# Kernel tuning notes

Measured on AMD Instinct MI355X. Metric: run time of the kernel, lower is better.

The kernel has to match this reference:

```python
import jax, jax.numpy as jnp
import numpy as np

N, E, F0, HEADS, B, OUT = 100000, 1600000, 128, 4, 64, 32
CHANNELS = [16, 8, 4, 2]
NEG_SLOPE = 0.2


def setup_inputs() -> dict:
    key = jax.random.key(0)
    ks = jax.random.split(key, 40)
    inp = {}
    inp['x'] = jax.random.normal(ks[0], (N, F0), dtype=jnp.float32)
    inp['edge_index'] = jax.random.randint(ks[1], (2, E), 0, N, dtype=jnp.int64)
    inp['batch'] = jnp.sort(jax.random.randint(ks[2], (N,), 0, B, dtype=jnp.int64))
    # GATConv params per layer: W [in, heads*out], att_src/att_dst [heads, out], bias [heads*out]
    in_dim = F0
    ki = 3
    for li, oc in enumerate(CHANNELS, start=1):
        scale = 1.0 / np.sqrt(in_dim)
        inp[f'W{li}'] = jax.random.normal(ks[ki], (in_dim, HEADS * oc), dtype=jnp.float32) * scale
        inp[f'a_src{li}'] = jax.random.normal(ks[ki + 1], (HEADS, oc), dtype=jnp.float32) * 0.1
        inp[f'a_dst{li}'] = jax.random.normal(ks[ki + 2], (HEADS, oc), dtype=jnp.float32) * 0.1
        inp[f'b{li}'] = jnp.zeros((HEADS * oc,), dtype=jnp.float32)
        ki += 3
        in_dim = HEADS * oc
    inp['W_fc'] = jax.random.normal(ks[ki], (2 * HEADS, OUT), dtype=jnp.float32) * (1.0 / np.sqrt(2 * HEADS))
    inp['b_fc'] = jnp.zeros((OUT,), dtype=jnp.float32)
    return inp


def gat_layer(x, src, dst, W, a_src, a_dst, b, oc):
    n = x.shape[0]
    h = (x @ W).reshape(n, HEADS, oc)                    # [N, H, C]
    al_s = jnp.einsum('nhc,hc->nh', h, a_src)            # [N, H]
    al_d = jnp.einsum('nhc,hc->nh', h, a_dst)
    e = jax.nn.leaky_relu(al_s[src] + al_d[dst], NEG_SLOPE)  # [E, H]
    # segment softmax over incoming edges per destination node
    m = jax.ops.segment_max(e, dst, num_segments=n)
    m = jnp.where(jnp.isfinite(m), m, 0.0)
    ex = jnp.exp(e - m[dst])
    s = jax.ops.segment_sum(ex, dst, num_segments=n)
    alpha = ex / (s[dst] + 1e-16)                        # [E, H]
    out = jax.ops.segment_sum(h[src] * alpha[:, :, None], dst, num_segments=n)
    return out.reshape(n, HEADS * oc) + b


def reference(x, edge_index, batch, W1, a_src1, a_dst1, b1, W2, a_src2, a_dst2, b2,
              W3, a_src3, a_dst3, b3, W4, a_src4, a_dst4, b4, W_fc, b_fc):
    n = x.shape[0]
    loops = jnp.arange(n, dtype=edge_index.dtype)
    src = jnp.concatenate([edge_index[0], loops])   # PyG GATConv adds self-loops
    dst = jnp.concatenate([edge_index[1], loops])
    params = [(W1, a_src1, a_dst1, b1), (W2, a_src2, a_dst2, b2),
              (W3, a_src3, a_dst3, b3), (W4, a_src4, a_dst4, b4)]
    h = x
    for (W, a_s, a_d, b), oc in zip(params, CHANNELS):
        h = jax.nn.relu(gat_layer(h, src, dst, W, a_s, a_d, b, oc))
        # dropout(0.3) is identity at inference
    # global mean pool over graphs in the batch
    sums = jax.ops.segment_sum(h, batch, num_segments=B)
    cnt = jax.ops.segment_sum(jnp.ones((n,), h.dtype), batch, num_segments=B)
    pooled = sums / jnp.maximum(cnt, 1.0)[:, None]
    return pooled @ W_fc + b_fc
```

## Files before the change

### kernel.cpp

```cpp
#include <hip/hip_runtime.h>
#include <hip/hip_bf16.h>

#define NNODES 100000
#define NEDGES 1600000
#define NHEADS 4
#define NGRAPH 64
#define NOUTF  32
#define BSH    9
#define NBUK   ((NNODES + 511) >> 9)
#define BPAD   16
#define BCAP   9216
#define CGRID  512
#define G1GRID ((NNODES + 63) / 64)

__device__ __forceinline__ unsigned short f2bf(float f) {
    union { float f; unsigned u; } v;
    v.f = f;
    unsigned r = v.u + 0x7FFF + ((v.u >> 16) & 1);
    return (unsigned short)(r >> 16);
}
__device__ __forceinline__ float bflo(unsigned u) {
    union { unsigned u; float f; } v;
    v.u = u << 16;
    return v.f;
}
__device__ __forceinline__ float bfhi(unsigned u) {
    union { unsigned u; float f; } v;
    v.u = u & 0xFFFF0000u;
    return v.f;
}

__device__ __forceinline__ bool ei_is_int64(const int* __restrict__ ei) {
    int acc = 0;
    #pragma unroll
    for (int i = 0; i < 32; i++) acc |= ei[2 * i + 1];
    return acc == 0;
}

__device__ __forceinline__ void fma4(float4& a, float s, const float4& b) {
    a.x += s * b.x;
    a.y += s * b.y;
    a.z += s * b.z;
    a.w += s * b.w;
}

__global__ __launch_bounds__(256) void gat_coarse_gemm1_kernel(
        const int* __restrict__ ei, const int* __restrict__ bt,
        int* __restrict__ bkcur, int* __restrict__ packed, int* __restrict__ bat,
        const float* __restrict__ x, const float* __restrict__ W1,
        const float* __restrict__ as1, const float* __restrict__ ad1,
        unsigned short* __restrict__ h1, float* __restrict__ al_s,
        float* __restrict__ al_d, int ne, int n) {
    __shared__ float smem[64 * 64 + 64 * 132];
    const int tid = threadIdx.x;
    if (blockIdx.x < CGRID) {
        int* hist = (int*)smem;
        int* base = hist + NBUK;
        for (int i = tid; i < NBUK; i += 256) hist[i] = 0;
        __syncthreads();
        bool wide = ei_is_int64(ei);
        int chunk = (ne + CGRID - 1) / CGRID;
        int e0 = blockIdx.x * chunk;
        int e1 = min(e0 + chunk, ne);
        for (int i = e0 + tid; i < e1; i += 256) {
            int d = wide ? ei[2 * (ne + i)] : ei[ne + i];
            atomicAdd(&hist[d >> BSH], 1);
        }
        __syncthreads();
        for (int i = tid; i < NBUK; i += 256)
            base[i] = hist[i] ? atomicAdd(&bkcur[i * BPAD], hist[i]) : 0;
        __syncthreads();
        for (int i = tid; i < NBUK; i += 256) hist[i] = 0;
        __syncthreads();
        for (int i = e0 + tid; i < e1; i += 256) {
            int s = wide ? ei[2 * i] : ei[i];
            int d = wide ? ei[2 * (ne + i)] : ei[ne + i];
            int bk = d >> BSH;
            int pos = base[bk] + atomicAdd(&hist[bk], 1);
            if (pos < BCAP) packed[bk * BCAP + pos] = s | ((d & 511) << 17);
        }
        int gid = blockIdx.x * 256 + tid;
        for (int i = gid; i < n; i += CGRID * 256) bat[i] = wide ? bt[2 * i] : bt[i];
    } else {
        constexpr int DIN = 128, DOUT = 64, KTILE = 64;
        constexpr int OG = DOUT / 4;
        constexpr int NPB = 64;
        constexpr int S = DIN + 4;
        constexpr int C = DOUT / NHEADS;
        float* Wl = smem;
        float* xs = smem + KTILE * DOUT;
        const int base = (blockIdx.x - CGRID) * NPB;
        constexpr int KC = DIN / 4;
        for (int i = tid; i < NPB * KC; i += 256) {
            int nn = i / KC, kc = i - nn * KC;
            int nd = base + nn;
            float4 v = (nd < n) ? ((const float4*)x)[(size_t)nd * KC + kc]
                                : make_float4(0.f, 0.f, 0.f, 0.f);
            *(float4*)&xs[nn * S + kc * 4] = v;
        }
        const int og = tid % OG;
        const int ng = tid / OG;
        const int n0 = ng * 4;
        float4 acc[4] = {};
        for (int kt = 0; kt < DIN; kt += KTILE) {
            __syncthreads();
            for (int i = tid; i < KTILE * OG; i += 256)
                ((float4*)Wl)[i] = ((const float4*)W1)[kt * OG + i];
            __syncthreads();
            #pragma unroll 2
            for (int k = 0; k < KTILE; k += 4) {
                float4 wv[4], xv[4];
                #pragma unroll
                for (int j = 0; j < 4; j++)
                    wv[j] = *(const float4*)&Wl[(k + j) * DOUT + og * 4];
                #pragma unroll
                for (int r = 0; r < 4; r++)
                    xv[r] = *(const float4*)&xs[(n0 + r) * S + kt + k];
                #pragma unroll
                for (int r = 0; r < 4; r++) {
                    fma4(acc[r], xv[r].x, wv[0]);
                    fma4(acc[r], xv[r].y, wv[1]);
                    fma4(acc[r], xv[r].z, wv[2]);
                    fma4(acc[r], xv[r].w, wv[3]);
                }
            }
        }
        float4 asv = ((const float4*)as1)[og];
        float4 adv = ((const float4*)ad1)[og];
        #pragma unroll
        for (int r = 0; r < 4; r++) {
            int node = base + n0 + r;
            bool ok = node < n;
            if (ok) {
                ushort4 o;
                o.x = f2bf(acc[r].x);
                o.y = f2bf(acc[r].y);
                o.z = f2bf(acc[r].z);
                o.w = f2bf(acc[r].w);
                ((ushort4*)h1)[(size_t)node * OG + og] = o;
            }
            float ps = acc[r].x * asv.x + acc[r].y * asv.y + acc[r].z * asv.z + acc[r].w * asv.w;
            float pd = acc[r].x * adv.x + acc[r].y * adv.y + acc[r].z * adv.z + acc[r].w * adv.w;
            #pragma unroll
            for (int off = 1; off < C / 4; off <<= 1) {
                ps += __shfl_xor(ps, off);
                pd += __shfl_xor(pd, off);
            }
            if (ok && (og % (C / 4)) == 0) {
                int hh = og / (C / 4);
                al_s[node * NHEADS + hh] = ps;
                al_d[node * NHEADS + hh] = pd;
            }
        }
    }
}

__global__ __launch_bounds__(256) void gat_fine_kernel(
        const int* __restrict__ packed, const int* __restrict__ bkcur,
        int* __restrict__ row_ptr, int* __restrict__ col, int n) {
    __shared__ int bscan[256];
    __shared__ int dg[512];
    __shared__ int excl[512];
    __shared__ int partial[256];
    __shared__ int cur[512];
    int b = blockIdx.x;
    int tid = threadIdx.x;
    int c = (tid < NBUK) ? bkcur[tid * BPAD] : 0;
    bscan[tid] = c;
    __syncthreads();
    for (int off = 1; off < 256; off <<= 1) {
        int u = (tid >= off) ? bscan[tid - off] : 0;
        __syncthreads();
        bscan[tid] += u;
        __syncthreads();
    }
    int cntb = bkcur[b * BPAD];
    int csr0 = bscan[b] - cntb;
    for (int i = tid; i < 512; i += 256) dg[i] = 0;
    __syncthreads();
    int pbeg = b * BCAP;
    int pend = pbeg + cntb;
    for (int t = pbeg + tid; t < pend; t += 256)
        atomicAdd(&dg[packed[t] >> 17], 1);
    __syncthreads();
    int a0 = dg[2 * tid], a1 = dg[2 * tid + 1];
    int s = a0 + a1;
    partial[tid] = s;
    __syncthreads();
    for (int off = 1; off < 256; off <<= 1) {
        int u = (tid >= off) ? partial[tid - off] : 0;
        __syncthreads();
        partial[tid] += u;
        __syncthreads();
    }
    int ebase = partial[tid] - s;
    excl[2 * tid] = ebase;
    excl[2 * tid + 1] = ebase + a0;
    cur[2 * tid] = ebase;
    cur[2 * tid + 1] = ebase + a0;
    __syncthreads();
    int node0 = b << BSH;
    for (int i = tid; i < 512; i += 256) {
        int nd = node0 + i;
        if (nd < n) row_ptr[nd] = csr0 + excl[i];
    }
    if (b == NBUK - 1 && tid == 0) row_ptr[n] = bscan[NBUK - 1];
    for (int t = pbeg + tid; t < pend; t += 256) {
        int v = packed[t];
        int pos = atomicAdd(&cur[v >> 17], 1);
        col[csr0 + pos] = v & 0x1FFFF;
    }
}

template<int DIN, int DOUT, int KTILE, bool BF16OUT>
__global__ __launch_bounds__(256) void gat_gemm_attn_kernel(
        const float* __restrict__ in, const float* __restrict__ W,
        const float* __restrict__ a_src, const float* __restrict__ a_dst,
        void* __restrict__ hout, float* __restrict__ al_s, float* __restrict__ al_d, int n) {
    constexpr int OG = DOUT / 4;
    constexpr int NPB = 1024 / OG;
    constexpr int S = DIN + 4;
    constexpr int C = DOUT / NHEADS;
    __shared__ float Wl[KTILE * DOUT];
    __shared__ float xs[NPB * S];
    const int tid = threadIdx.x;
    const int base = blockIdx.x * NPB;
    constexpr int KC = DIN / 4;
    for (int i = tid; i < NPB * KC; i += 256) {
        int nn = i / KC, kc = i - nn * KC;
        int nd = base + nn;
        float4 v = (nd < n) ? ((const float4*)in)[(size_t)nd * KC + kc]
                            : make_float4(0.f, 0.f, 0.f, 0.f);
        *(float4*)&xs[nn * S + kc * 4] = v;
    }
    const int og = tid % OG;
    const int ng = tid / OG;
    const int n0 = ng * 4;
    float4 acc[4] = {};
    for (int kt = 0; kt < DIN; kt += KTILE) {
        __syncthreads();
        for (int i = tid; i < KTILE * OG; i += 256)
            ((float4*)Wl)[i] = ((const float4*)W)[kt * OG + i];
        __syncthreads();
        #pragma unroll 2
        for (int k = 0; k < KTILE; k += 4) {
            float4 wv[4], xv[4];
            #pragma unroll
            for (int j = 0; j < 4; j++)
                wv[j] = *(const float4*)&Wl[(k + j) * DOUT + og * 4];
            #pragma unroll
            for (int r = 0; r < 4; r++)
                xv[r] = *(const float4*)&xs[(n0 + r) * S + kt + k];
            #pragma unroll
            for (int r = 0; r < 4; r++) {
                fma4(acc[r], xv[r].x, wv[0]);
                fma4(acc[r], xv[r].y, wv[1]);
                fma4(acc[r], xv[r].z, wv[2]);
                fma4(acc[r], xv[r].w, wv[3]);
            }
        }
    }
    float4 asv = ((const float4*)a_src)[og];
    float4 adv = ((const float4*)a_dst)[og];
    #pragma unroll
    for (int r = 0; r < 4; r++) {
        int node = base + n0 + r;
        bool ok = node < n;
        if (ok) {
            if constexpr (BF16OUT) {
                ushort4 o;
                o.x = f2bf(acc[r].x);
                o.y = f2bf(acc[r].y);
                o.z = f2bf(acc[r].z);
                o.w = f2bf(acc[r].w);
                ((ushort4*)hout)[(size_t)node * OG + og] = o;
            } else {
                ((float4*)hout)[(size_t)node * OG + og] = acc[r];
            }
        }
        if constexpr (C >= 4) {
            float ps = acc[r].x * asv.x + acc[r].y * asv.y + acc[r].z * asv.z + acc[r].w * asv.w;
            float pd = acc[r].x * adv.x + acc[r].y * adv.y + acc[r].z * adv.z + acc[r].w * adv.w;
            #pragma unroll
            for (int off = 1; off < C / 4; off <<= 1) {
                ps += __shfl_xor(ps, off);
                pd += __shfl_xor(pd, off);
            }
            if (ok && (og % (C / 4)) == 0) {
                int hh = og / (C / 4);
                al_s[node * NHEADS + hh] = ps;
                al_d[node * NHEADS + hh] = pd;
            }
        } else {
            if (ok) {
                al_s[node * NHEADS + 2 * og]     = acc[r].x * asv.x + acc[r].y * asv.y;
                al_s[node * NHEADS + 2 * og + 1] = acc[r].z * asv.z + acc[r].w * asv.w;
                al_d[node * NHEADS + 2 * og]     = acc[r].x * adv.x + acc[r].y * adv.y;
                al_d[node * NHEADS + 2 * og + 1] = acc[r].z * adv.z + acc[r].w * adv.w;
            }
        }
    }
}

template<int C>
__global__ __launch_bounds__(256) void gat_agg_bf16_kernel(
        const unsigned short* __restrict__ h, const float* __restrict__ al_s,
        const float* __restrict__ al_d, const int* __restrict__ row_ptr,
        const int* __restrict__ col, const float* __restrict__ bias,
        float* __restrict__ out, int n) {
    constexpr int G = NHEADS * C;
    constexpr int L = G / 8;
    constexpr int NG = 64 / L;
    int lane = threadIdx.x & 63;
    int node = blockIdx.x * 4 + (threadIdx.x >> 6);
    if (node >= n) return;
    int sub = lane & (L - 1);
    int g = lane / L;
    int hh = (sub * 8) / C;
    int beg = row_ptr[node];
    int cnt = row_ptr[node + 1] - beg;
    float ald = al_d[node * NHEADS + hh];
    const uint4* h4 = (const uint4*)h;
    float a[8] = {};
    float ws = 0.f;
    for (int t = g; t < cnt + 1; t += NG) {
        int src = (t < cnt) ? col[beg + t] : node;
        float e = al_s[src * NHEADS + hh] + ald;
        e = (e > 0.f) ? e : 0.2f * e;
        float w = __expf(e);
        uint4 hv = h4[(size_t)src * L + sub];
        ws += w;
        a[0] += w * bflo(hv.x);
        a[1] += w * bfhi(hv.x);
        a[2] += w * bflo(hv.y);
        a[3] += w * bfhi(hv.y);
        a[4] += w * bflo(hv.z);
        a[5] += w * bfhi(hv.z);
        a[6] += w * bflo(hv.w);
        a[7] += w * bfhi(hv.w);
    }
    #pragma unroll
    for (int off = L; off < 64; off <<= 1) {
        #pragma unroll
        for (int k = 0; k < 8; k++) a[k] += __shfl_xor(a[k], off);
        ws += __shfl_xor(ws, off);
    }
    if (g == 0) {
        float inv = 1.f / (ws + 1e-16f);
        int j0 = sub * 8;
        float4 o0, o1;
        float4 bv0 = *(const float4*)&bias[j0];
        float4 bv1 = *(const float4*)&bias[j0 + 4];
        o0.x = a[0] * inv + bv0.x;
        o0.y = a[1] * inv + bv0.y;
        o0.z = a[2] * inv + bv0.z;
        o0.w = a[3] * inv + bv0.w;
        o1.x = a[4] * inv + bv1.x;
        o1.y = a[5] * inv + bv1.y;
        o1.z = a[6] * inv + bv1.z;
        o1.w = a[7] * inv + bv1.w;
        o0.x = (o0.x > 0.f) ? o0.x : 0.f;
        o0.y = (o0.y > 0.f) ? o0.y : 0.f;
        o0.z = (o0.z > 0.f) ? o0.z : 0.f;
        o0.w = (o0.w > 0.f) ? o0.w : 0.f;
        o1.x = (o1.x > 0.f) ? o1.x : 0.f;
        o1.y = (o1.y > 0.f) ? o1.y : 0.f;
        o1.z = (o1.z > 0.f) ? o1.z : 0.f;
        o1.w = (o1.w > 0.f) ? o1.w : 0.f;
        *(float4*)&out[(size_t)node * G + j0] = o0;
        *(float4*)&out[(size_t)node * G + j0 + 4] = o1;
    }
}

__global__ __launch_bounds__(256) void gat_agg_bf16_c4_kernel(
        const unsigned short* __restrict__ h, const float* __restrict__ al_s,
        const float* __restrict__ al_d, const int* __restrict__ row_ptr,
        const int* __restrict__ col, const float* __restrict__ bias,
        float* __restrict__ out, int n) {
    constexpr int G = 16;
    constexpr int L = 4;
    constexpr int NG = 16;
    int lane = threadIdx.x & 63;
    int node = blockIdx.x * 4 + (threadIdx.x >> 6);
    if (node >= n) return;
    int sub = lane & (L - 1);
    int g = lane / L;
    int beg = row_ptr[node];
    int cnt = row_ptr[node + 1] - beg;
    float ald = al_d[node * NHEADS + sub];
    const uint2* h2 = (const uint2*)h;
    float a[4] = {};
    float ws = 0.f;
    for (int t = g; t < cnt + 1; t += NG) {
        int src = (t < cnt) ? col[beg + t] : node;
        float e = al_s[src * NHEADS + sub] + ald;
        e = (e > 0.f) ? e : 0.2f * e;
        float w = __expf(e);
        uint2 hv = h2[(size_t)src * L + sub];
        ws += w;
        a[0] += w * bflo(hv.x);
        a[1] += w * bfhi(hv.x);
        a[2] += w * bflo(hv.y);
        a[3] += w * bfhi(hv.y);
    }
    #pragma unroll
    for (int off = L; off < 64; off <<= 1) {
        #pragma unroll
        for (int k = 0; k < 4; k++) a[k] += __shfl_xor(a[k], off);
        ws += __shfl_xor(ws, off);
    }
    if (g == 0) {
        float inv = 1.f / (ws + 1e-16f);
        int j0 = sub * 4;
        float4 bv = *(const float4*)&bias[j0];
        float4 o;
        o.x = a[0] * inv + bv.x;
        o.y = a[1] * inv + bv.y;
        o.z = a[2] * inv + bv.z;
        o.w = a[3] * inv + bv.w;
        o.x = (o.x > 0.f) ? o.x : 0.f;
        o.y = (o.y > 0.f) ? o.y : 0.f;
        o.z = (o.z > 0.f) ? o.z : 0.f;
        o.w = (o.w > 0.f) ? o.w : 0.f;
        *(float4*)&out[(size_t)node * G + j0] = o;
    }
}

template<int C>
__global__ __launch_bounds__(256) void gat_agg_kernel(
        const float* __restrict__ h, const float* __restrict__ al_s, const float* __restrict__ al_d,
        const int* __restrict__ row_ptr, const int* __restrict__ col,
        const float* __restrict__ bias, float* __restrict__ out, int n) {
    constexpr int G = NHEADS * C;
    constexpr int L = G / 4;
    constexpr int NG = 64 / L;
    int lane = threadIdx.x & 63;
    int node = blockIdx.x * 4 + (threadIdx.x >> 6);
    if (node >= n) return;
    int sub = lane & (L - 1);
    int g = lane / L;
    int c0 = sub * 4;
    int beg = row_ptr[node];
    int cnt = row_ptr[node + 1] - beg;
    float ald0 = al_d[node * NHEADS + c0 / C];
    float ald1 = al_d[node * NHEADS + (c0 + 2) / C];
    const float4* h4 = (const float4*)h;
    float4 acc = make_float4(0.f, 0.f, 0.f, 0.f);
    float ws0 = 0.f, ws1 = 0.f;
    for (int t = g; t < cnt + 1; t += NG) {
        int src = (t < cnt) ? col[beg + t] : node;
        float4 hv = h4[src * L + sub];
        float e0 = al_s[src * NHEADS + c0 / C] + ald0;
        float e1 = al_s[src * NHEADS + (c0 + 2) / C] + ald1;
        e0 = (e0 > 0.f) ? e0 : 0.2f * e0;
        e1 = (e1 > 0.f) ? e1 : 0.2f * e1;
        float w0 = __expf(e0);
        float w1 = __expf(e1);
        ws0 += w0;
        ws1 += w1;
        acc.x += w0 * hv.x;
        acc.y += w0 * hv.y;
        acc.z += w1 * hv.z;
        acc.w += w1 * hv.w;
    }
    #pragma unroll
    for (int off = L; off < 64; off <<= 1) {
        acc.x += __shfl_xor(acc.x, off);
        acc.y += __shfl_xor(acc.y, off);
        acc.z += __shfl_xor(acc.z, off);
        acc.w += __shfl_xor(acc.w, off);
        ws0 += __shfl_xor(ws0, off);
        ws1 += __shfl_xor(ws1, off);
    }
    if (g == 0) {
        float4 bv = ((const float4*)bias)[sub];
        float4 v;
        v.x = acc.x / (ws0 + 1e-16f) + bv.x;
        v.y = acc.y / (ws0 + 1e-16f) + bv.y;
        v.z = acc.z / (ws1 + 1e-16f) + bv.z;
        v.w = acc.w / (ws1 + 1e-16f) + bv.w;
        v.x = (v.x > 0.f) ? v.x : 0.f;
        v.y = (v.y > 0.f) ? v.y : 0.f;
        v.z = (v.z > 0.f) ? v.z : 0.f;
        v.w = (v.w > 0.f) ? v.w : 0.f;
        ((float4*)out)[node * L + sub] = v;
    }
}

__global__ __launch_bounds__(256) void gat_poolfc_kernel(
        const float* __restrict__ x, const int* __restrict__ bat,
        const float* __restrict__ Wfc, const float* __restrict__ bfc,
        float* __restrict__ out, int n) {
    __shared__ float sh[256][9];
    int b = blockIdx.x;
    int tid = threadIdx.x;
    int lo = 0, hi = n;
    while (lo < hi) { int mid = (lo + hi) >> 1; if (bat[mid] < b) lo = mid + 1; else hi = mid; }
    int i0 = lo;
    hi = n;
    while (lo < hi) { int mid = (lo + hi) >> 1; if (bat[mid] < b + 1) lo = mid + 1; else hi = mid; }
    int i1 = lo;
    float a[8] = {};
    for (int i = i0 + tid; i < i1; i += 256) {
        float4 v0 = ((const float4*)x)[(size_t)i * 2];
        float4 v1 = ((const float4*)x)[(size_t)i * 2 + 1];
        a[0] += v0.x; a[1] += v0.y; a[2] += v0.z; a[3] += v0.w;
        a[4] += v1.x; a[5] += v1.y; a[6] += v1.z; a[7] += v1.w;
    }
    #pragma unroll
    for (int k = 0; k < 8; k++) sh[tid][k] = a[k];
    __syncthreads();
    for (int off = 128; off >= 1; off >>= 1) {
        if (tid < off)
            #pragma unroll
            for (int k = 0; k < 8; k++) sh[tid][k] += sh[tid + off][k];
        __syncthreads();
    }
    if (tid < NOUTF) {
        float c = (float)(i1 - i0);
        if (c < 1.f) c = 1.f;
        float acc = bfc[tid];
        #pragma unroll
        for (int d = 0; d < 8; d++) acc += (sh[0][d] / c) * Wfc[d * NOUTF + tid];
        out[b * NOUTF + tid] = acc;
    }
}

extern "C" void kernel_launch(void* const* d_in, const int* in_sizes, int n_in,
                              void* d_out, int out_size, void* d_ws, size_t ws_size,
                              hipStream_t stream) {
    const float* x = (const float*)d_in[0];
    const int* ei = (const int*)d_in[1];
    const int* batch = (const int*)d_in[2];
    const float* W1 = (const float*)d_in[3];
    const float* as1 = (const float*)d_in[4];
    const float* ad1 = (const float*)d_in[5];
    const float* b1 = (const float*)d_in[6];
    const float* W2 = (const float*)d_in[7];
    const float* as2 = (const float*)d_in[8];
    const float* ad2 = (const float*)d_in[9];
    const float* b2 = (const float*)d_in[10];
    const float* W3 = (const float*)d_in[11];
    const float* as3 = (const float*)d_in[12];
    const float* ad3 = (const float*)d_in[13];
    const float* b3 = (const float*)d_in[14];
    const float* W4 = (const float*)d_in[15];
    const float* as4 = (const float*)d_in[16];
    const float* ad4 = (const float*)d_in[17];
    const float* b4 = (const float*)d_in[18];
    const float* Wfc = (const float*)d_in[19];
    const float* bfc = (const float*)d_in[20];

    const int n = NNODES, ne = NEDGES;

    char* p = (char*)d_ws;
    auto carve = [&](size_t bytes) {
        char* r = p;
        p += (bytes + 255) & ~(size_t)255;
        return r;
    };
    int* row_ptr = (int*)carve((size_t)(n + 1) * 4);
    int* col = (int*)carve((size_t)ne * 4);
    int* bkcur = (int*)carve(256 * BPAD * 4);
    int* packed = (int*)carve((size_t)NBUK * BCAP * 4);
    float* buf_h = (float*)carve((size_t)n * 64 * 4);
    float* buf_x = (float*)carve((size_t)n * 64 * 4);
    float* al_s = (float*)carve((size_t)n * NHEADS * 4);
    float* al_d = (float*)carve((size_t)n * NHEADS * 4);
    int* bat = (int*)carve((size_t)n * 4);
    unsigned short* h_bf16 = (unsigned short*)buf_h;

    hipMemsetAsync(bkcur, 0, 256 * BPAD * 4, stream);

    gat_coarse_gemm1_kernel<<<CGRID + G1GRID, 256, 0, stream>>>(
        ei, batch, bkcur, packed, bat, x, W1, as1, ad1, h_bf16, al_s, al_d, ne, n);

    gat_fine_kernel<<<NBUK, 256, 0, stream>>>(packed, bkcur, row_ptr, col, n);

    gat_agg_bf16_kernel<16><<<(n + 3) / 4, 256, 0, stream>>>(
        h_bf16, al_s, al_d, row_ptr, col, b1, buf_x, n);

    gat_gemm_attn_kernel<64, 32, 64, true><<<(n + 127) / 128, 256, 0, stream>>>(
        buf_x, W2, as2, ad2, h_bf16, al_s, al_d, n);
    gat_agg_bf16_kernel<8><<<(n + 3) / 4, 256, 0, stream>>>(
        h_bf16, al_s, al_d, row_ptr, col, b2, buf_x, n);

    gat_gemm_attn_kernel<32, 16, 32, true><<<(n + 255) / 256, 256, 0, stream>>>(
        buf_x, W3, as3, ad3, h_bf16, al_s, al_d, n);
    gat_agg_bf16_c4_kernel<<<(n + 3) / 4, 256, 0, stream>>>(
        h_bf16, al_s, al_d, row_ptr, col, b3, buf_x, n);

    gat_gemm_attn_kernel<16, 8, 16, false><<<(n + 511) / 512, 256, 0, stream>>>(
        buf_x, W4, as4, ad4, buf_h, al_s, al_d, n);
    gat_agg_kernel<2><<<(n + 3) / 4, 256, 0, stream>>>(buf_h, al_s, al_d, row_ptr, col, b4, buf_x, n);

    gat_poolfc_kernel<<<NGRAPH, 256, 0, stream>>>(buf_x, bat, Wfc, bfc, (float*)d_out, n);
}
```

Baseline: 409.1 us.

## Map aggregation to thread groups per node and widen CSR fine kernel

The aggregation kernels now give each destination node a small group of lanes (L lanes covering the feature row), so a wave handles many nodes, instead of one wave per node with an edge-parallel shuffle reduction. Each lane walks all incoming edges itself, two per iteration, which removes the cross-lane shuffle reductions and the idle lanes on low-degree nodes. The cost is serial per-lane loops, so high-degree nodes cause imbalance and divergence within a wave. The fine CSR build kernel also goes to 1024 threads to speed up its histogram and scatter loops.

```diff
diff --git a/kernel.cpp b/kernel.cpp
--- a/kernel.cpp
+++ b/kernel.cpp
@@ -155,7 +155,7 @@
     }
 }
 
-__global__ __launch_bounds__(256) void gat_fine_kernel(
+__global__ __launch_bounds__(1024) void gat_fine_kernel(
         const int* __restrict__ packed, const int* __restrict__ bkcur,
         int* __restrict__ row_ptr, int* __restrict__ col, int n) {
     __shared__ int bscan[256];
@@ -165,47 +165,51 @@
     __shared__ int cur[512];
     int b = blockIdx.x;
     int tid = threadIdx.x;
-    int c = (tid < NBUK) ? bkcur[tid * BPAD] : 0;
-    bscan[tid] = c;
+    if (tid < 256) bscan[tid] = (tid < NBUK) ? bkcur[tid * BPAD] : 0;
+    if (tid < 512) dg[tid] = 0;
     __syncthreads();
     for (int off = 1; off < 256; off <<= 1) {
-        int u = (tid >= off) ? bscan[tid - off] : 0;
-        __syncthreads();
-        bscan[tid] += u;
+        int u = (tid < 256 && tid >= off) ? bscan[tid - off] : 0;
+        __syncthreads();
+        if (tid < 256) bscan[tid] += u;
         __syncthreads();
     }
     int cntb = bkcur[b * BPAD];
     int csr0 = bscan[b] - cntb;
-    for (int i = tid; i < 512; i += 256) dg[i] = 0;
-    __syncthreads();
     int pbeg = b * BCAP;
     int pend = pbeg + cntb;
-    for (int t = pbeg + tid; t < pend; t += 256)
+    for (int t = pbeg + tid; t < pend; t += 1024)
         atomicAdd(&dg[packed[t] >> 17], 1);
     __syncthreads();
-    int a0 = dg[2 * tid], a1 = dg[2 * tid + 1];
-    int s = a0 + a1;
-    partial[tid] = s;
+    int a0 = 0, a1 = 0, s = 0;
+    if (tid < 256) {
+        a0 = dg[2 * tid];
+        a1 = dg[2 * tid + 1];
+        s = a0 + a1;
+        partial[tid] = s;
+    }
     __syncthreads();
     for (int off = 1; off < 256; off <<= 1) {
-        int u = (tid >= off) ? partial[tid - off] : 0;
-        __syncthreads();
-        partial[tid] += u;
-        __syncthreads();
-    }
-    int ebase = partial[tid] - s;
-    excl[2 * tid] = ebase;
-    excl[2 * tid + 1] = ebase + a0;
-    cur[2 * tid] = ebase;
-    cur[2 * tid + 1] = ebase + a0;
+        int u = (tid < 256 && tid >= off) ? partial[tid - off] : 0;
+        __syncthreads();
+        if (tid < 256) partial[tid] += u;
+        __syncthreads();
+    }
+    if (tid < 256) {
+        int ebase = partial[tid] - s;
+        excl[2 * tid] = ebase;
+        excl[2 * tid + 1] = ebase + a0;
+        cur[2 * tid] = ebase;
+        cur[2 * tid + 1] = ebase + a0;
+    }
     __syncthreads();
     int node0 = b << BSH;
-    for (int i = tid; i < 512; i += 256) {
-        int nd = node0 + i;
-        if (nd < n) row_ptr[nd] = csr0 + excl[i];
+    if (tid < 512) {
+        int nd = node0 + tid;
+        if (nd < n) row_ptr[nd] = csr0 + excl[tid];
     }
     if (b == NBUK - 1 && tid == 0) row_ptr[n] = bscan[NBUK - 1];
-    for (int t = pbeg + tid; t < pend; t += 256) {
+    for (int t = pbeg + tid; t < pend; t += 1024) {
         int v = packed[t];
         int pos = atomicAdd(&cur[v >> 17], 1);
         col[csr0 + pos] = v & 0x1FFFF;
@@ -302,189 +306,243 @@
     }
 }
 
-template<int C>
-__global__ __launch_bounds__(256) void gat_agg_bf16_kernel(
+template<int G>
+__global__ __launch_bounds__(256) void gat_agg_group_kernel(
         const unsigned short* __restrict__ h, const float* __restrict__ al_s,
         const float* __restrict__ al_d, const int* __restrict__ row_ptr,
         const int* __restrict__ col, const float* __restrict__ bias,
         float* __restrict__ out, int n) {
-    constexpr int G = NHEADS * C;
     constexpr int L = G / 8;
-    constexpr int NG = 64 / L;
+    constexpr int PW = 64 / L;
+    constexpr int C = G / NHEADS;
     int lane = threadIdx.x & 63;
-    int node = blockIdx.x * 4 + (threadIdx.x >> 6);
+    int sub = lane & (L - 1);
+    int gidx = lane / L;
+    int node = blockIdx.x * (4 * PW) + (threadIdx.x >> 6) * PW + gidx;
     if (node >= n) return;
-    int sub = lane & (L - 1);
-    int g = lane / L;
-    int hh = (sub * 8) / C;
     int beg = row_ptr[node];
     int cnt = row_ptr[node + 1] - beg;
-    float ald = al_d[node * NHEADS + hh];
     const uint4* h4 = (const uint4*)h;
-    float a[8] = {};
-    float ws = 0.f;
-    for (int t = g; t < cnt + 1; t += NG) {
-        int src = (t < cnt) ? col[beg + t] : node;
-        float e = al_s[src * NHEADS + hh] + ald;
-        e = (e > 0.f) ? e : 0.2f * e;
-        float w = __expf(e);
-        uint4 hv = h4[(size_t)src * L + sub];
-        ws += w;
-        a[0] += w * bflo(hv.x);
-        a[1] += w * bfhi(hv.x);
-        a[2] += w * bflo(hv.y);
-        a[3] += w * bfhi(hv.y);
-        a[4] += w * bflo(hv.z);
-        a[5] += w * bfhi(hv.z);
-        a[6] += w * bflo(hv.w);
-        a[7] += w * bfhi(hv.w);
-    }
-    #pragma unroll
-    for (int off = L; off < 64; off <<= 1) {
+    float acc[8] = {};
+    int j0 = sub * 8;
+    if constexpr (C >= 8) {
+        const int hh = (sub * 8) / C;
+        float ald = al_d[node * NHEADS + hh];
+        float ws = 0.f;
+        int total = cnt + 1;
+        int t = 0;
+        for (; t + 2 <= total; t += 2) {
+            int s0 = col[beg + t];
+            int s1 = (t + 1 < cnt) ? col[beg + t + 1] : node;
+            float e0 = al_s[s0 * NHEADS + hh] + ald;
+            float e1 = al_s[s1 * NHEADS + hh] + ald;
+            uint4 hv0 = h4[(size_t)s0 * L + sub];
+            uint4 hv1 = h4[(size_t)s1 * L + sub];
+            e0 = (e0 > 0.f) ? e0 : 0.2f * e0;
+            e1 = (e1 > 0.f) ? e1 : 0.2f * e1;
+            float w0 = __expf(e0);
+            float w1 = __expf(e1);
+            ws += w0;
+            acc[0] += w0 * bflo(hv0.x);
+            acc[1] += w0 * bfhi(hv0.x);
+            acc[2] += w0 * bflo(hv0.y);
+            acc[3] += w0 * bfhi(hv0.y);
+            acc[4] += w0 * bflo(hv0.z);
+            acc[5] += w0 * bfhi(hv0.z);
+            acc[6] += w0 * bflo(hv0.w);
+            acc[7] += w0 * bfhi(hv0.w);
+            ws += w1;
+            acc[0] += w1 * bflo(hv1.x);
+            acc[1] += w1 * bfhi(hv1.x);
+            acc[2] += w1 * bflo(hv1.y);
+            acc[3] += w1 * bfhi(hv1.y);
+            acc[4] += w1 * bflo(hv1.z);
+            acc[5] += w1 * bfhi(hv1.z);
+            acc[6] += w1 * bflo(hv1.w);
+            acc[7] += w1 * bfhi(hv1.w);
+        }
+        if (t < total) {
+            int s0 = (t < cnt) ? col[beg + t] : node;
+            float e0 = al_s[s0 * NHEADS + hh] + ald;
+            uint4 hv0 = h4[(size_t)s0 * L + sub];
+            e0 = (e0 > 0.f) ? e0 : 0.2f * e0;
+            float w0 = __expf(e0);
+            ws += w0;
+            acc[0] += w0 * bflo(hv0.x);
+            acc[1] += w0 * bfhi(hv0.x);
+            acc[2] += w0 * bflo(hv0.y);
+            acc[3] += w0 * bfhi(hv0.y);
+            acc[4] += w0 * bflo(hv0.z);
+            acc[5] += w0 * bfhi(hv0.z);
+            acc[6] += w0 * bflo(hv0.w);
+            acc[7] += w0 * bfhi(hv0.w);
+        }
+        float inv = 1.f / (ws + 1e-16f);
         #pragma unroll
-        for (int k = 0; k < 8; k++) a[k] += __shfl_xor(a[k], off);
-        ws += __shfl_xor(ws, off);
-    }
-    if (g == 0) {
-        float inv = 1.f / (ws + 1e-16f);
-        int j0 = sub * 8;
-        float4 o0, o1;
-        float4 bv0 = *(const float4*)&bias[j0];
-        float4 bv1 = *(const float4*)&bias[j0 + 4];
-        o0.x = a[0] * inv + bv0.x;
-        o0.y = a[1] * inv + bv0.y;
-        o0.z = a[2] * inv + bv0.z;
-        o0.w = a[3] * inv + bv0.w;
-        o1.x = a[4] * inv + bv1.x;
-        o1.y = a[5] * inv + bv1.y;
-        o1.z = a[6] * inv + bv1.z;
-        o1.w = a[7] * inv + bv1.w;
-        o0.x = (o0.x > 0.f) ? o0.x : 0.f;
-        o0.y = (o0.y > 0.f) ? o0.y : 0.f;
-        o0.z = (o0.z > 0.f) ? o0.z : 0.f;
-        o0.w = (o0.w > 0.f) ? o0.w : 0.f;
-        o1.x = (o1.x > 0.f) ? o1.x : 0.f;
-        o1.y = (o1.y > 0.f) ? o1.y : 0.f;
-        o1.z = (o1.z > 0.f) ? o1.z : 0.f;
-        o1.w = (o1.w > 0.f) ? o1.w : 0.f;
-        *(float4*)&out[(size_t)node * G + j0] = o0;
-        *(float4*)&out[(size_t)node * G + j0 + 4] = o1;
-    }
-}
-
-__global__ __launch_bounds__(256) void gat_agg_bf16_c4_kernel(
-        const unsigned short* __restrict__ h, const float* __restrict__ al_s,
-        const float* __restrict__ al_d, const int* __restrict__ row_ptr,
-        const int* __restrict__ col, const float* __restrict__ bias,
-        float* __restrict__ out, int n) {
-    constexpr int G = 16;
-    constexpr int L = 4;
-    constexpr int NG = 16;
-    int lane = threadIdx.x & 63;
-    int node = blockIdx.x * 4 + (threadIdx.x >> 6);
-    if (node >= n) return;
-    int sub = lane & (L - 1);
-    int g = lane / L;
-    int beg = row_ptr[node];
-    int cnt = row_ptr[node + 1] - beg;
-    float ald = al_d[node * NHEADS + sub];
-    const uint2* h2 = (const uint2*)h;
-    float a[4] = {};
-    float ws = 0.f;
-    for (int t = g; t < cnt + 1; t += NG) {
-        int src = (t < cnt) ? col[beg + t] : node;
-        float e = al_s[src * NHEADS + sub] + ald;
-        e = (e > 0.f) ? e : 0.2f * e;
-        float w = __expf(e);
-        uint2 hv = h2[(size_t)src * L + sub];
-        ws += w;
-        a[0] += w * bflo(hv.x);
-        a[1] += w * bfhi(hv.x);
-        a[2] += w * bflo(hv.y);
-        a[3] += w * bfhi(hv.y);
-    }
-    #pragma unroll
-    for (int off = L; off < 64; off <<= 1) {
+        for (int k = 0; k < 8; k++) acc[k] = acc[k] * inv + bias[j0 + k];
+    } else {
+        const int hh0 = 2 * sub, hh1 = 2 * sub + 1;
+        float ald0 = al_d[node * NHEADS + hh0];
+        float ald1 = al_d[node * NHEADS + hh1];
+        float ws0 = 0.f, ws1 = 0.f;
+        int total = cnt + 1;
+        int t = 0;
+        for (; t + 2 <= total; t += 2) {
+            int s0 = col[beg + t];
+            int s1 = (t + 1 < cnt) ? col[beg + t + 1] : node;
+            float e00 = al_s[s0 * NHEADS + hh0] + ald0;
+            float e01 = al_s[s0 * NHEADS + hh1] + ald1;
+            float e10 = al_s[s1 * NHEADS + hh0] + ald0;
+            float e11 = al_s[s1 * NHEADS + hh1] + ald1;
+            uint4 hv0 = h4[(size_t)s0 * L + sub];
+            uint4 hv1 = h4[(size_t)s1 * L + sub];
+            e00 = (e00 > 0.f) ? e00 : 0.2f * e00;
+            e01 = (e01 > 0.f) ? e01 : 0.2f * e01;
+            e10 = (e10 > 0.f) ? e10 : 0.2f * e10;
+            e11 = (e11 > 0.f) ? e11 : 0.2f * e11;
+            float w00 = __expf(e00);
+            float w01 = __expf(e01);
+            float w10 = __expf(e10);
+            float w11 = __expf(e11);
+            ws0 += w00;
+            ws1 += w01;
+            acc[0] += w00 * bflo(hv0.x);
+            acc[1] += w00 * bfhi(hv0.x);
+            acc[2] += w00 * bflo(hv0.y);
+            acc[3] += w00 * bfhi(hv0.y);
+            acc[4] += w01 * bflo(hv0.z);
+            acc[5] += w01 * bfhi(hv0.z);
+            acc[6] += w01 * bflo(hv0.w);
+            acc[7] += w01 * bfhi(hv0.w);
+            ws0 += w10;
+            ws1 += w11;
+            acc[0] += w10 * bflo(hv1.x);
+            acc[1] += w10 * bfhi(hv1.x);
+            acc[2] += w10 * bflo(hv1.y);
+            acc[3] += w10 * bfhi(hv1.y);
+            acc[4] += w11 * bflo(hv1.z);
+            acc[5] += w11 * bfhi(hv1.z);
+            acc[6] += w11 * bflo(hv1.w);
+            acc[7] += w11 * bfhi(hv1.w);
+        }
+        if (t < total) {
+            int s0 = (t < cnt) ? col[beg + t] : node;
+            float e00 = al_s[s0 * NHEADS + hh0] + ald0;
+            float e01 = al_s[s0 * NHEADS + hh1] + ald1;
+            uint4 hv0 = h4[(size_t)s0 * L + sub];
+            e00 = (e00 > 0.f) ? e00 : 0.2f * e00;
+            e01 = (e01 > 0.f) ? e01 : 0.2f * e01;
+            float w00 = __expf(e00);
+            float w01 = __expf(e01);
+            ws0 += w00;
+            ws1 += w01;
+            acc[0] += w00 * bflo(hv0.x);
+            acc[1] += w00 * bfhi(hv0.x);
+            acc[2] += w00 * bflo(hv0.y);
+            acc[3] += w00 * bfhi(hv0.y);
+            acc[4] += w01 * bflo(hv0.z);
+            acc[5] += w01 * bfhi(hv0.z);
+            acc[6] += w01 * bflo(hv0.w);
+            acc[7] += w01 * bfhi(hv0.w);
+        }
+        float inv0 = 1.f / (ws0 + 1e-16f);
+        float inv1 = 1.f / (ws1 + 1e-16f);
         #pragma unroll
-        for (int k = 0; k < 4; k++) a[k] += __shfl_xor(a[k], off);
-        ws += __shfl_xor(ws, off);
-    }
-    if (g == 0) {
-        float inv = 1.f / (ws + 1e-16f);
-        int j0 = sub * 4;
-        float4 bv = *(const float4*)&bias[j0];
-        float4 o;
-        o.x = a[0] * inv + bv.x;
-        o.y = a[1] * inv + bv.y;
-        o.z = a[2] * inv + bv.z;
-        o.w = a[3] * inv + bv.w;
-        o.x = (o.x > 0.f) ? o.x : 0.f;
-        o.y = (o.y > 0.f) ? o.y : 0.f;
-        o.z = (o.z > 0.f) ? o.z : 0.f;
-        o.w = (o.w > 0.f) ? o.w : 0.f;
-        *(float4*)&out[(size_t)node * G + j0] = o;
-    }
-}
-
-template<int C>
-__global__ __launch_bounds__(256) void gat_agg_kernel(
+        for (int k = 0; k < 4; k++) acc[k] = acc[k] * inv0 + bias[j0 + k];
+        #pragma unroll
+        for (int k = 4; k < 8; k++) acc[k] = acc[k] * inv1 + bias[j0 + k];
+    }
+    float4 o0, o1;
+    o0.x = (acc[0] > 0.f) ? acc[0] : 0.f;
+    o0.y = (acc[1] > 0.f) ? acc[1] : 0.f;
+    o0.z = (acc[2] > 0.f) ? acc[2] : 0.f;
+    o0.w = (acc[3] > 0.f) ? acc[3] : 0.f;
+    o1.x = (acc[4] > 0.f) ? acc[4] : 0.f;
+    o1.y = (acc[5] > 0.f) ? acc[5] : 0.f;
+    o1.z = (acc[6] > 0.f) ? acc[6] : 0.f;
+    o1.w = (acc[7] > 0.f) ? acc[7] : 0.f;
+    *(float4*)&out[(size_t)node * G + j0] = o0;
+    *(float4*)&out[(size_t)node * G + j0 + 4] = o1;
+}
+
+__global__ __launch_bounds__(256) void gat_agg_f32_group_kernel(
         const float* __restrict__ h, const float* __restrict__ al_s, const float* __restrict__ al_d,
         const int* __restrict__ row_ptr, const int* __restrict__ col,
         const float* __restrict__ bias, float* __restrict__ out, int n) {
-    constexpr int G = NHEADS * C;
-    constexpr int L = G / 4;
-    constexpr int NG = 64 / L;
+    constexpr int L = 2;
+    constexpr int PW = 32;
     int lane = threadIdx.x & 63;
-    int node = blockIdx.x * 4 + (threadIdx.x >> 6);
+    int sub = lane & 1;
+    int gidx = lane >> 1;
+    int node = blockIdx.x * (4 * PW) + (threadIdx.x >> 6) * PW + gidx;
     if (node >= n) return;
-    int sub = lane & (L - 1);
-    int g = lane / L;
-    int c0 = sub * 4;
     int beg = row_ptr[node];
     int cnt = row_ptr[node + 1] - beg;
-    float ald0 = al_d[node * NHEADS + c0 / C];
-    float ald1 = al_d[node * NHEADS + (c0 + 2) / C];
+    const int hh0 = 2 * sub, hh1 = 2 * sub + 1;
+    float ald0 = al_d[node * NHEADS + hh0];
+    float ald1 = al_d[node * NHEADS + hh1];
     const float4* h4 = (const float4*)h;
     float4 acc = make_float4(0.f, 0.f, 0.f, 0.f);
     float ws0 = 0.f, ws1 = 0.f;
-    for (int t = g; t < cnt + 1; t += NG) {
-        int src = (t < cnt) ? col[beg + t] : node;
-        float4 hv = h4[src * L + sub];
-        float e0 = al_s[src * NHEADS + c0 / C] + ald0;
-        float e1 = al_s[src * NHEADS + (c0 + 2) / C] + ald1;
-        e0 = (e0 > 0.f) ? e0 : 0.2f * e0;
-        e1 = (e1 > 0.f) ? e1 : 0.2f * e1;
-        float w0 = __expf(e0);
-        float w1 = __expf(e1);
-        ws0 += w0;
-        ws1 += w1;
-        acc.x += w0 * hv.x;
-        acc.y += w0 * hv.y;
-        acc.z += w1 * hv.z;
-        acc.w += w1 * hv.w;
-    }
-    #pragma unroll
-    for (int off = L; off < 64; off <<= 1) {
-        acc.x += __shfl_xor(acc.x, off);
-        acc.y += __shfl_xor(acc.y, off);
-        acc.z += __shfl_xor(acc.z, off);
-        acc.w += __shfl_xor(acc.w, off);
-        ws0 += __shfl_xor(ws0, off);
-        ws1 += __shfl_xor(ws1, off);
-    }
-    if (g == 0) {
-        float4 bv = ((const float4*)bias)[sub];
-        float4 v;
-        v.x = acc.x / (ws0 + 1e-16f) + bv.x;
-        v.y = acc.y / (ws0 + 1e-16f) + bv.y;
-        v.z = acc.z / (ws1 + 1e-16f) + bv.z;
-        v.w = acc.w / (ws1 + 1e-16f) + bv.w;
-        v.x = (v.x > 0.f) ? v.x : 0.f;
-        v.y = (v.y > 0.f) ? v.y : 0.f;
-        v.z = (v.z > 0.f) ? v.z : 0.f;
-        v.w = (v.w > 0.f) ? v.w : 0.f;
-        ((float4*)out)[node * L + sub] = v;
-    }
+    int total = cnt + 1;
+    int t = 0;
+    for (; t + 2 <= total; t += 2) {
+        int s0 = col[beg + t];
+        int s1 = (t + 1 < cnt) ? col[beg + t + 1] : node;
+        float e00 = al_s[s0 * NHEADS + hh0] + ald0;
+        float e01 = al_s[s0 * NHEADS + hh1] + ald1;
+        float e10 = al_s[s1 * NHEADS + hh0] + ald0;
+        float e11 = al_s[s1 * NHEADS + hh1] + ald1;
+        float4 hv0 = h4[(size_t)s0 * L + sub];
+        float4 hv1 = h4[(size_t)s1 * L + sub];
+        e00 = (e00 > 0.f) ? e00 : 0.2f * e00;
+        e01 = (e01 > 0.f) ? e01 : 0.2f * e01;
+        e10 = (e10 > 0.f) ? e10 : 0.2f * e10;
+        e11 = (e11 > 0.f) ? e11 : 0.2f * e11;
+        float w00 = __expf(e00);
+        float w01 = __expf(e01);
+        float w10 = __expf(e10);
+        float w11 = __expf(e11);
+        ws0 += w00;
+        ws1 += w01;
+        acc.x += w00 * hv0.x;
+        acc.y += w00 * hv0.y;
+        acc.z += w01 * hv0.z;
+        acc.w += w01 * hv0.w;
+        ws0 += w10;
+        ws1 += w11;
+        acc.x += w10 * hv1.x;
+        acc.y += w10 * hv1.y;
+        acc.z += w11 * hv1.z;
+        acc.w += w11 * hv1.w;
+    }
+    if (t < total) {
+        int s0 = (t < cnt) ? col[beg + t] : node;
+        float e00 = al_s[s0 * NHEADS + hh0] + ald0;
+        float e01 = al_s[s0 * NHEADS + hh1] + ald1;
+        float4 hv0 = h4[(size_t)s0 * L + sub];
+        e00 = (e00 > 0.f) ? e00 : 0.2f * e00;
+        e01 = (e01 > 0.f) ? e01 : 0.2f * e01;
+        float w00 = __expf(e00);
+        float w01 = __expf(e01);
+        ws0 += w00;
+        ws1 += w01;
+        acc.x += w00 * hv0.x;
+        acc.y += w00 * hv0.y;
+        acc.z += w01 * hv0.z;
+        acc.w += w01 * hv0.w;
+    }
+    float4 bv = ((const float4*)bias)[sub];
+    float4 v;
+    v.x = acc.x / (ws0 + 1e-16f) + bv.x;
+    v.y = acc.y / (ws0 + 1e-16f) + bv.y;
+    v.z = acc.z / (ws1 + 1e-16f) + bv.z;
+    v.w = acc.w / (ws1 + 1e-16f) + bv.w;
+    v.x = (v.x > 0.f) ? v.x : 0.f;
+    v.y = (v.y > 0.f) ? v.y : 0.f;
+    v.z = (v.z > 0.f) ? v.z : 0.f;
+    v.w = (v.w > 0.f) ? v.w : 0.f;
+    ((float4*)out)[(size_t)node * L + sub] = v;
 }
 
 __global__ __launch_bounds__(256) void gat_poolfc_kernel(
@@ -575,24 +633,25 @@
     gat_coarse_gemm1_kernel<<<CGRID + G1GRID, 256, 0, stream>>>(
         ei, batch, bkcur, packed, bat, x, W1, as1, ad1, h_bf16, al_s, al_d, ne, n);
 
-    gat_fine_kernel<<<NBUK, 256, 0, stream>>>(packed, bkcur, row_ptr, col, n);
-
-    gat_agg_bf16_kernel<16><<<(n + 3) / 4, 256, 0, stream>>>(
+    gat_fine_kernel<<<NBUK, 1024, 0, stream>>>(packed, bkcur, row_ptr, col, n);
+
+    gat_agg_group_kernel<64><<<(n + 31) / 32, 256, 0, stream>>>(
         h_bf16, al_s, al_d, row_ptr, col, b1, buf_x, n);
 
     gat_gemm_attn_kernel<64, 32, 64, true><<<(n + 127) / 128, 256, 0, stream>>>(
         buf_x, W2, as2, ad2, h_bf16, al_s, al_d, n);
-    gat_agg_bf16_kernel<8><<<(n + 3) / 4, 256, 0, stream>>>(
+    gat_agg_group_kernel<32><<<(n + 63) / 64, 256, 0, stream>>>(
         h_bf16, al_s, al_d, row_ptr, col, b2, buf_x, n);
 
     gat_gemm_attn_kernel<32, 16, 32, true><<<(n + 255) / 256, 256, 0, stream>>>(
         buf_x, W3, as3, ad3, h_bf16, al_s, al_d, n);
-    gat_agg_bf16_c4_kernel<<<(n + 3) / 4, 256, 0, stream>>>(
+    gat_agg_group_kernel<16><<<(n + 127) / 128, 256, 0, stream>>>(
         h_bf16, al_s, al_d, row_ptr, col, b3, buf_x, n);
 
     gat_gemm_attn_kernel<16, 8, 16, false><<<(n + 511) / 512, 256, 0, stream>>>(
         buf_x, W4, as4, ad4, buf_h, al_s, al_d, n);
-    gat_agg_kernel<2><<<(n + 3) / 4, 256, 0, stream>>>(buf_h, al_s, al_d, row_ptr, col, b4, buf_x, n);
+    gat_agg_f32_group_kernel<<<(n + 127) / 128, 256, 0, stream>>>(
+        buf_h, al_s, al_d, row_ptr, col, b4, buf_x, n);
 
     gat_poolfc_kernel<<<NGRAPH, 256, 0, stream>>>(buf_x, bat, Wfc, bfc, (float*)d_out, n);
 }
```

After: 386.2 us. 5.6% less time.
